# Performance work log

Measured on AMD Instinct MI355X. Metric: run time of the kernel, lower is better.

## Reference

```python
import jax, jax.numpy as jnp
import numpy as np

E = 8_000_000  # n_edges
B = 4096       # n_graphs

def setup_inputs() -> dict:
    key = jax.random.key(0)
    ks = jax.random.split(key, 9)
    src = jax.random.normal(ks[0], (E, 1), dtype=jnp.float32)
    dest = jax.random.normal(ks[1], (E, 1), dtype=jnp.float32)
    edge_attr = jax.random.normal(ks[2], (E, 1), dtype=jnp.float32)
    u = jax.random.normal(ks[3], (B, 1), dtype=jnp.float32)
    batch = jax.random.randint(ks[4], (E,), 0, B, dtype=jnp.int64)
    # edge_mlp params: Lin(4,10) -> ReLU -> Lin(10,19)
    W1 = jax.random.normal(ks[5], (4, 10), dtype=jnp.float32) * (1.0 / np.sqrt(4))
    b1 = jnp.zeros((10,), dtype=jnp.float32)
    W2 = jax.random.normal(ks[6], (10, 19), dtype=jnp.float32) * (1.0 / np.sqrt(10))
    b2 = jnp.zeros((19,), dtype=jnp.float32)
    return {"src": src, "dest": dest, "edge_attr": edge_attr, "u": u,
            "batch": batch, "W1": W1, "b1": b1, "W2": W2, "b2": b2}

def reference(src, dest, edge_attr, u, batch, W1, b1, W2, b2):
    # gather per-graph global state to edges, concat along feature dim
    x = jnp.concatenate([src, dest, edge_attr, u[batch]], axis=1)  # [E, 4]
    h = jax.nn.relu(x @ W1 + b1)                                   # [E, 10]
    return h @ W2 + b2                                             # [E, 19]
```

## Files before the change

kernel.cpp:

```cpp
#include <hip/hip_runtime.h>

#define THREADS 256
#define F_HID 10
#define F_OUT 19

__global__ __launch_bounds__(THREADS) void edge_mlp_kernel(
    const float* __restrict__ src,
    const float* __restrict__ dst,
    const float* __restrict__ ea,
    const float* __restrict__ u,
    const int*   __restrict__ batch,
    const float* __restrict__ W1,
    const float* __restrict__ b1,
    const float* __restrict__ W2,
    const float* __restrict__ b2,
    float* __restrict__ out,
    int n_edges)
{
    __shared__ float lds[THREADS * F_OUT];

    const int tid = threadIdx.x;
    const int e   = blockIdx.x * THREADS + tid;

    float o[F_OUT];
    if (e < n_edges) {
        const float x0 = src[e];
        const float x1 = dst[e];
        const float x2 = ea[e];
        const float x3 = u[batch[e]];

        #pragma unroll
        for (int k = 0; k < F_OUT; ++k) o[k] = b2[k];

        #pragma unroll
        for (int j = 0; j < F_HID; ++j) {
            float a = b1[j];
            a = fmaf(x0, W1[0 * F_HID + j], a);
            a = fmaf(x1, W1[1 * F_HID + j], a);
            a = fmaf(x2, W1[2 * F_HID + j], a);
            a = fmaf(x3, W1[3 * F_HID + j], a);
            a = fmaxf(a, 0.0f);
            #pragma unroll
            for (int k = 0; k < F_OUT; ++k)
                o[k] = fmaf(a, W2[j * F_OUT + k], o[k]);
        }
    } else {
        #pragma unroll
        for (int k = 0; k < F_OUT; ++k) o[k] = 0.0f;
    }

    #pragma unroll
    for (int k = 0; k < F_OUT; ++k) lds[tid * F_OUT + k] = o[k];
    __syncthreads();

    const int block_start = blockIdx.x * THREADS;
    const int base = block_start * F_OUT;
    int valid = n_edges - block_start;
    if (valid >= THREADS) {
        float4* __restrict__ outv = (float4*)(out + base);
        const float4* __restrict__ ldsv = (const float4*)lds;
        #pragma unroll
        for (int idx = tid; idx < (THREADS * F_OUT) / 4; idx += THREADS)
            outv[idx] = ldsv[idx];
    } else {
        const int nflt = valid * F_OUT;
        for (int idx = tid; idx < nflt; idx += THREADS)
            out[base + idx] = lds[idx];
    }
}

extern "C" void kernel_launch(void* const* d_in, const int* in_sizes, int n_in,
                              void* d_out, int out_size, void* d_ws, size_t ws_size,
                              hipStream_t stream) {
    const float* src   = (const float*)d_in[0];
    const float* dst   = (const float*)d_in[1];
    const float* ea    = (const float*)d_in[2];
    const float* u     = (const float*)d_in[3];
    const int*   batch = (const int*)  d_in[4];
    const float* W1    = (const float*)d_in[5];
    const float* b1    = (const float*)d_in[6];
    const float* W2    = (const float*)d_in[7];
    const float* b2    = (const float*)d_in[8];
    float* out = (float*)d_out;

    const int n = in_sizes[0];
    const int blocks = (n + THREADS - 1) / THREADS;
    edge_mlp_kernel<<<blocks, THREADS, 0, stream>>>(
        src, dst, ea, u, batch, W1, b1, W2, b2, out, n);
}
```

Measured before the change: 696.9 us.

## Process two edges per thread with per-wave LDS slabs and nontemporal stores

Each thread now computes two edges, loading inputs with 2-wide vector loads, and reuses each W2 weight across both edges. The block-wide LDS transpose and __syncthreads are replaced by per-wave slabs synchronized with a wave barrier. Output is written with nontemporal float4 stores. The goal is to cut load instructions and sync overhead on a store-bandwidth-bound kernel, at the cost of more registers and fewer blocks.

```diff
diff --git a/kernel.cpp b/kernel.cpp
--- a/kernel.cpp
+++ b/kernel.cpp
@@ -1,8 +1,40 @@
 #include <hip/hip_runtime.h>
 
 #define THREADS 256
-#define F_HID 10
-#define F_OUT 19
+#define EPT     2
+#define F_HID   10
+#define F_OUT   19
+#define WAVEW   64
+#define EPW     (WAVEW * EPT)
+#define SLAB    (EPW * F_OUT)
+#define NW      (THREADS / WAVEW)
+
+typedef float f32x2 __attribute__((ext_vector_type(2)));
+typedef float f32x4 __attribute__((ext_vector_type(4)));
+typedef int   i32x2 __attribute__((ext_vector_type(2)));
+
+__device__ __forceinline__ void mlp1(float x0, float x1, float x2, float x3,
+                                     const float* __restrict__ W1,
+                                     const float* __restrict__ b1,
+                                     const float* __restrict__ W2,
+                                     const float* __restrict__ b2,
+                                     float* __restrict__ o)
+{
+    #pragma unroll
+    for (int k = 0; k < F_OUT; ++k) o[k] = b2[k];
+    #pragma unroll
+    for (int j = 0; j < F_HID; ++j) {
+        float a = b1[j];
+        a = fmaf(x0, W1[0 * F_HID + j], a);
+        a = fmaf(x1, W1[1 * F_HID + j], a);
+        a = fmaf(x2, W1[2 * F_HID + j], a);
+        a = fmaf(x3, W1[3 * F_HID + j], a);
+        a = fmaxf(a, 0.0f);
+        #pragma unroll
+        for (int k = 0; k < F_OUT; ++k)
+            o[k] = fmaf(a, W2[j * F_OUT + k], o[k]);
+    }
+}
 
 __global__ __launch_bounds__(THREADS) void edge_mlp_kernel(
     const float* __restrict__ src,
@@ -17,55 +49,86 @@
     float* __restrict__ out,
     int n_edges)
 {
-    __shared__ float lds[THREADS * F_OUT];
+    __shared__ float lds[NW * SLAB];
 
-    const int tid = threadIdx.x;
-    const int e   = blockIdx.x * THREADS + tid;
+    const int tid  = threadIdx.x;
+    const int lane = tid & (WAVEW - 1);
+    const int wv   = tid >> 6;
+    const int bs   = blockIdx.x * (THREADS * EPT);
 
-    float o[F_OUT];
-    if (e < n_edges) {
-        const float x0 = src[e];
-        const float x1 = dst[e];
-        const float x2 = ea[e];
-        const float x3 = u[batch[e]];
+    if (bs + THREADS * EPT <= n_edges) {
+        const int e0 = bs + wv * EPW + lane * EPT;
 
+        const f32x2 xs = *(const f32x2*)(src + e0);
+        const f32x2 xd = *(const f32x2*)(dst + e0);
+        const f32x2 xa = *(const f32x2*)(ea  + e0);
+        const i32x2 bi = *(const i32x2*)(batch + e0);
+        f32x2 xu; xu.x = u[bi.x]; xu.y = u[bi.y];
+
+        float o[EPT * F_OUT];
         #pragma unroll
-        for (int k = 0; k < F_OUT; ++k) o[k] = b2[k];
+        for (int k = 0; k < F_OUT; ++k) { o[k] = b2[k]; o[F_OUT + k] = b2[k]; }
 
         #pragma unroll
         for (int j = 0; j < F_HID; ++j) {
-            float a = b1[j];
-            a = fmaf(x0, W1[0 * F_HID + j], a);
-            a = fmaf(x1, W1[1 * F_HID + j], a);
-            a = fmaf(x2, W1[2 * F_HID + j], a);
-            a = fmaf(x3, W1[3 * F_HID + j], a);
-            a = fmaxf(a, 0.0f);
+            const float w0 = W1[0 * F_HID + j];
+            const float w1 = W1[1 * F_HID + j];
+            const float w2 = W1[2 * F_HID + j];
+            const float w3 = W1[3 * F_HID + j];
+            const float bb = b1[j];
+
+            float a0 = fmaf(xu.x, w3, bb);
+            a0 = fmaf(xa.x, w2, a0);
+            a0 = fmaf(xd.x, w1, a0);
+            a0 = fmaf(xs.x, w0, a0);
+            a0 = fmaxf(a0, 0.0f);
+
+            float a1 = fmaf(xu.y, w3, bb);
+            a1 = fmaf(xa.y, w2, a1);
+            a1 = fmaf(xd.y, w1, a1);
+            a1 = fmaf(xs.y, w0, a1);
+            a1 = fmaxf(a1, 0.0f);
+
             #pragma unroll
-            for (int k = 0; k < F_OUT; ++k)
-                o[k] = fmaf(a, W2[j * F_OUT + k], o[k]);
+            for (int k = 0; k < F_OUT; ++k) {
+                const float w = W2[j * F_OUT + k];
+                o[k]         = fmaf(a0, w, o[k]);
+                o[F_OUT + k] = fmaf(a1, w, o[F_OUT + k]);
+            }
+        }
+
+        float* slab = lds + wv * SLAB;
+        {
+            f32x2* my = (f32x2*)(slab + lane * (EPT * F_OUT));
+            #pragma unroll
+            for (int p = 0; p < (EPT * F_OUT) / 2; ++p) {
+                f32x2 t;
+                t.x = o[2 * p];
+                t.y = o[2 * p + 1];
+                my[p] = t;
+            }
+        }
+        __builtin_amdgcn_wave_barrier();
+
+        {
+            const f32x4* sv = (const f32x4*)slab;
+            f32x4* ov = (f32x4*)(out + (size_t)(bs + wv * EPW) * F_OUT);
+            for (int idx = lane; idx < SLAB / 4; idx += WAVEW)
+                __builtin_nontemporal_store(sv[idx], ov + idx);
         }
     } else {
+        const int e0 = bs + wv * EPW + lane * EPT;
         #pragma unroll
-        for (int k = 0; k < F_OUT; ++k) o[k] = 0.0f;
-    }
-
-    #pragma unroll
-    for (int k = 0; k < F_OUT; ++k) lds[tid * F_OUT + k] = o[k];
-    __syncthreads();
-
-    const int block_start = blockIdx.x * THREADS;
-    const int base = block_start * F_OUT;
-    int valid = n_edges - block_start;
-    if (valid >= THREADS) {
-        float4* __restrict__ outv = (float4*)(out + base);
-        const float4* __restrict__ ldsv = (const float4*)lds;
-        #pragma unroll
-        for (int idx = tid; idx < (THREADS * F_OUT) / 4; idx += THREADS)
-            outv[idx] = ldsv[idx];
-    } else {
-        const int nflt = valid * F_OUT;
-        for (int idx = tid; idx < nflt; idx += THREADS)
-            out[base + idx] = lds[idx];
+        for (int r = 0; r < EPT; ++r) {
+            const int e = e0 + r;
+            if (e < n_edges) {
+                float o[F_OUT];
+                mlp1(src[e], dst[e], ea[e], u[batch[e]], W1, b1, W2, b2, o);
+                #pragma unroll
+                for (int k = 0; k < F_OUT; ++k)
+                    out[(size_t)e * F_OUT + k] = o[k];
+            }
+        }
     }
 }
 
@@ -84,7 +147,8 @@
     float* out = (float*)d_out;
 
     const int n = in_sizes[0];
-    const int blocks = (n + THREADS - 1) / THREADS;
+    const int edges_per_block = THREADS * EPT;
+    const int blocks = (n + edges_per_block - 1) / edges_per_block;
     edge_mlp_kernel<<<blocks, THREADS, 0, stream>>>(
         src, dst, ea, u, batch, W1, b1, W2, b2, out, n);
 }
```

Result: no change. 701.8 us (+0.7%).
